# Performance work log

Measured on AMD Instinct MI355X. Metric: run time of the kernel, lower is better.

Reference implementation:

```python
import jax, jax.numpy as jnp
import numpy as np

N = 50000
E = 800000
IN_CH = 128
HID = 16
HEADS = 8
OUT_CH = 64
NEG_SLOPE = 0.2


def _gat_conv(x, src, dst, W, a_src, a_dst, b, heads, ch):
    # x: [N, F_in]; W: [F_in, heads*ch]; a_src/a_dst: [heads, ch]; b: [heads*ch] or [ch]
    n = x.shape[0]
    h = (x @ W).reshape(n, heads, ch)                      # [N, H, C]
    s = jnp.einsum('nhc,hc->nh', h, a_src)                 # [N, H]
    d = jnp.einsum('nhc,hc->nh', h, a_dst)                 # [N, H]
    e = jax.nn.leaky_relu(s[src] + d[dst], NEG_SLOPE)      # [E, H]
    # numerically stable segment softmax over destination neighborhoods
    m = jax.ops.segment_max(e, dst, num_segments=n)        # [N, H]
    m = jnp.where(jnp.isfinite(m), m, 0.0)                 # guard isolated nodes
    w = jnp.exp(e - m[dst])                                # [E, H]
    z = jax.ops.segment_sum(w, dst, num_segments=n)        # [N, H]
    alpha = w / (z[dst] + 1e-16)                           # [E, H]
    msg = h[src] * alpha[:, :, None]                       # [E, H, C]
    out = jax.ops.segment_sum(msg, dst, num_segments=n)    # [N, H, C]
    return out.reshape(n, heads * ch) + b


def setup_inputs() -> dict:
    key = jax.random.key(0)
    ks = jax.random.split(key, 10)
    x = jax.random.normal(ks[0], (N, IN_CH), dtype=jnp.float32)
    edge_index = jax.random.randint(ks[1], (2, E), 0, N, dtype=jnp.int64)
    g1 = 1.0 / np.sqrt(IN_CH)
    g2 = 1.0 / np.sqrt(HEADS * HID)
    W1 = jax.random.normal(ks[2], (IN_CH, HEADS * HID), dtype=jnp.float32) * g1
    a_src1 = jax.random.normal(ks[3], (HEADS, HID), dtype=jnp.float32) * g2
    a_dst1 = jax.random.normal(ks[4], (HEADS, HID), dtype=jnp.float32) * g2
    b1 = jnp.zeros((HEADS * HID,), dtype=jnp.float32)
    W2 = jax.random.normal(ks[5], (HEADS * HID, OUT_CH), dtype=jnp.float32) * g2
    a_src2 = jax.random.normal(ks[6], (1, OUT_CH), dtype=jnp.float32) * (1.0 / np.sqrt(OUT_CH))
    a_dst2 = jax.random.normal(ks[7], (1, OUT_CH), dtype=jnp.float32) * (1.0 / np.sqrt(OUT_CH))
    b2 = jnp.zeros((OUT_CH,), dtype=jnp.float32)
    return {"x": x, "edge_index": edge_index,
            "W1": W1, "a_src1": a_src1, "a_dst1": a_dst1, "b1": b1,
            "W2": W2, "a_src2": a_src2, "a_dst2": a_dst2, "b2": b2}


def reference(x, edge_index, W1, a_src1, a_dst1, b1, W2, a_src2, a_dst2, b2):
    src, dst = edge_index[0], edge_index[1]
    # dropout layers are identity at inference
    h = _gat_conv(x, src, dst, W1, a_src1, a_dst1, b1, HEADS, HID)
    h = jax.nn.elu(h)
    out = _gat_conv(h, src, dst, W2, a_src2, a_dst2, b2, 1, OUT_CH)
    return out
```

## Files before the change

### kernel.cpp

```cpp
#include <hip/hip_runtime.h>
#include <hip/hip_fp16.h>

#define INCH   128
#define HEADS1 8
#define HID1   16
#define C1     128
#define C2     64
#define NEG_SLOPE 0.2f
#define SB     256

using f16x8 = __attribute__((ext_vector_type(8))) _Float16;
using f32x4 = __attribute__((ext_vector_type(4))) float;

__device__ __forceinline__ float lrelu(float v) { return v >= 0.f ? v : NEG_SLOPE * v; }
__device__ __forceinline__ int swzA(int row, int byteInRow) {
  return (row << 8) | (byteInRow ^ ((row & 15) << 4));
}


__global__ void prep_kernel(const float* __restrict__ x, __half* __restrict__ xh,
                            const float* __restrict__ W1, __half* __restrict__ W1t,
                            const float* __restrict__ W2, __half* __restrict__ W2t,
                            const int* __restrict__ dst, int* __restrict__ deg,
                            int cvtB, int tB, int total8, int E) {
  const int b = blockIdx.x, t = threadIdx.x;
  if (b < cvtB) {
    int i = b * 256 + t;
    if (i >= total8) return;
    const float4* p = (const float4*)x + (size_t)i * 2;
    float4 v0 = p[0], v1 = p[1];
    __half2 ha = __floats2half2_rn(v0.x, v0.y);
    __half2 hb = __floats2half2_rn(v0.z, v0.w);
    __half2 hc = __floats2half2_rn(v1.x, v1.y);
    __half2 hd = __floats2half2_rn(v1.z, v1.w);
    uint4 w = { *(unsigned*)&ha, *(unsigned*)&hb, *(unsigned*)&hc, *(unsigned*)&hd };
    ((uint4*)xh)[i] = w;
  } else if (b < cvtB + tB) {
    int id = (b - cvtB) * 256 + t;
    if (id < 128 * 128) {
      int col = id >> 7, k = id & 127;
      W1t[id] = __float2half(W1[k * 128 + col]);
    } else if (id < 128 * 128 + 64 * 128) {
      int idx = id - 128 * 128;
      int col = idx >> 7, k = idx & 127;
      W2t[idx] = __float2half(W2[k * 64 + col]);
    }
  } else {
    int e = (b - cvtB - tB) * 256 + t;
    if (e < E) atomicAdd(&deg[dst[e]], 1);
  }
}


__global__ void scan1_kernel(const int* __restrict__ deg, int* __restrict__ partial, int N) {
  __shared__ int sh[SB];
  const int b = blockIdx.x, t = threadIdx.x;
  const int chunk = (N + SB - 1) / SB;
  const int lo = b * chunk, hi = min(lo + chunk, N);
  int s = 0;
  for (int i = lo + t; i < hi; i += SB) s += deg[i];
  sh[t] = s;
  __syncthreads();
  for (int off = SB / 2; off; off >>= 1) {
    if (t < off) sh[t] += sh[t + off];
    __syncthreads();
  }
  if (t == 0) partial[b] = sh[0];
}

__global__ void scan3_kernel(const int* __restrict__ deg, const int* __restrict__ partial,
                             int* __restrict__ row_start, int N) {
  __shared__ int pref[SB];
  __shared__ int sh[SB];
  const int b = blockIdx.x, t = threadIdx.x;
  int pv = partial[t];
  pref[t] = pv;
  __syncthreads();
  for (int off = 1; off < SB; off <<= 1) {
    int u = (t >= off) ? pref[t - off] : 0;
    __syncthreads();
    pref[t] += u;
    __syncthreads();
  }
  const int chunk = (N + SB - 1) / SB;
  const int lo = b * chunk, hi = min(lo + chunk, N);
  int run = (b == 0) ? 0 : pref[b - 1];
  for (int base = lo; base < hi; base += SB) {
    int i = base + t;
    int v = (i < hi) ? deg[i] : 0;
    sh[t] = v;
    __syncthreads();
    for (int off = 1; off < SB; off <<= 1) {
      int u = (t >= off) ? sh[t - off] : 0;
      __syncthreads();
      sh[t] += u;
      __syncthreads();
    }
    if (i < hi) row_start[i] = run + sh[t] - v;
    run += sh[SB - 1];
    __syncthreads();
  }
  if (b == SB - 1 && t == 0) row_start[N] = run;
}

__global__ void fill_kernel(const int* __restrict__ src, const int* __restrict__ dst,
                            const int* __restrict__ row_start, int* __restrict__ cursor,
                            int* __restrict__ src_sorted, int E) {
  int e = blockIdx.x * blockDim.x + threadIdx.x;
  if (e >= E) return;
  int d = dst[e];
  int slot = row_start[d] + atomicAdd(&cursor[d], 1);
  src_sorted[slot] = src[e];
}

__global__ __launch_bounds__(256) void gemm1_mfma(
    const __half* __restrict__ xh, const __half* __restrict__ W1t,
    const float* __restrict__ a_src, const float* __restrict__ a_dst,
    __half* __restrict__ h1, float* __restrict__ s1, float* __restrict__ d1, int M) {
  __shared__ unsigned char As[16384];
  __shared__ unsigned char Bs[32768];
  const int t = threadIdx.x;
  const int m0 = blockIdx.x * 64;
  for (int c = t; c < 1024; c += 256) {
    int row = c >> 4, seg = c & 15;
    int gr = m0 + row;
    uint4 v = make_uint4(0, 0, 0, 0);
    if (gr < M) v = ((const uint4*)xh)[(unsigned)(gr << 4) + seg];
    *(uint4*)(As + swzA(row, seg << 4)) = v;
  }
  for (int c = t; c < 2048; c += 256) {
    int row = c >> 4, seg = c & 15;
    uint4 v = ((const uint4*)W1t)[(row << 4) + seg];
    *(uint4*)(Bs + swzA(row, seg << 4)) = v;
  }
  __syncthreads();
  const int l = t & 63, wid = t >> 6;
  const int c16 = l & 15;
  const int kOff = (l >> 4) << 4;
  const int rA = (wid << 4) | c16;
  f16x8 a[4];
#pragma unroll
  for (int kb = 0; kb < 4; ++kb)
    a[kb] = *(const f16x8*)(As + swzA(rA, (kb << 6) + kOff));
#pragma unroll
  for (int ct = 0; ct < 8; ++ct) {
    const int rB = (ct << 4) | c16;
    f32x4 acc = {0.f, 0.f, 0.f, 0.f};
#pragma unroll
    for (int kb = 0; kb < 4; ++kb) {
      f16x8 b = *(const f16x8*)(Bs + swzA(rB, (kb << 6) + kOff));
      acc = __builtin_amdgcn_mfma_f32_16x16x32_f16(a[kb], b, acc, 0, 0, 0);
    }
    const int colg = (ct << 4) + c16;
    const float asv = a_src[colg], adv = a_dst[colg];
#pragma unroll
    for (int i = 0; i < 4; ++i) {
      const int n = m0 + (wid << 4) + ((l >> 4) << 2) + i;
      float v = acc[i];
      float sv = v * asv, dv = v * adv;
      sv += __shfl_xor(sv, 1); sv += __shfl_xor(sv, 2);
      sv += __shfl_xor(sv, 4); sv += __shfl_xor(sv, 8);
      dv += __shfl_xor(dv, 1); dv += __shfl_xor(dv, 2);
      dv += __shfl_xor(dv, 4); dv += __shfl_xor(dv, 8);
      if (n < M) {
        h1[(unsigned)(n << 7) + colg] = __float2half(v);
        if (c16 == 0) { s1[n * HEADS1 + ct] = sv; d1[n * HEADS1 + ct] = dv; }
      }
    }
  }
}

__global__ __launch_bounds__(256) void gemm2_mfma(
    const __half* __restrict__ x2h, const __half* __restrict__ W2t,
    const float* __restrict__ a_src, const float* __restrict__ a_dst,
    __half* __restrict__ h2, float* __restrict__ s2, float* __restrict__ d2, int M) {
  __shared__ unsigned char As[16384];
  __shared__ unsigned char Bs[16384];
  const int t = threadIdx.x;
  const int m0 = blockIdx.x * 64;
  for (int c = t; c < 1024; c += 256) {
    int row = c >> 4, seg = c & 15;
    int gr = m0 + row;
    uint4 v = make_uint4(0, 0, 0, 0);
    if (gr < M) v = ((const uint4*)x2h)[(unsigned)(gr << 4) + seg];
    *(uint4*)(As + swzA(row, seg << 4)) = v;
  }
  for (int c = t; c < 1024; c += 256) {
    int row = c >> 4, seg = c & 15;
    uint4 v = ((const uint4*)W2t)[(row << 4) + seg];
    *(uint4*)(Bs + swzA(row, seg << 4)) = v;
  }
  __syncthreads();
  const int l = t & 63, wid = t >> 6;
  const int c16 = l & 15;
  const int kOff = (l >> 4) << 4;
  const int rA = (wid << 4) | c16;
  f16x8 a[4];
#pragma unroll
  for (int kb = 0; kb < 4; ++kb)
    a[kb] = *(const f16x8*)(As + swzA(rA, (kb << 6) + kOff));
  float svp[4] = {0.f, 0.f, 0.f, 0.f};
  float dvp[4] = {0.f, 0.f, 0.f, 0.f};
#pragma unroll
  for (int ct = 0; ct < 4; ++ct) {
    const int rB = (ct << 4) | c16;
    f32x4 acc = {0.f, 0.f, 0.f, 0.f};
#pragma unroll
    for (int kb = 0; kb < 4; ++kb) {
      f16x8 b = *(const f16x8*)(Bs + swzA(rB, (kb << 6) + kOff));
      acc = __builtin_amdgcn_mfma_f32_16x16x32_f16(a[kb], b, acc, 0, 0, 0);
    }
    const int colg = (ct << 4) + c16;
    const float asv = a_src[colg], adv = a_dst[colg];
#pragma unroll
    for (int i = 0; i < 4; ++i) {
      const int n = m0 + (wid << 4) + ((l >> 4) << 2) + i;
      float v = acc[i];
      svp[i] += v * asv;
      dvp[i] += v * adv;
      if (n < M) h2[(unsigned)(n << 6) + colg] = __float2half(v);
    }
  }
#pragma unroll
  for (int i = 0; i < 4; ++i) {
    float sv = svp[i], dv = dvp[i];
    sv += __shfl_xor(sv, 1); sv += __shfl_xor(sv, 2);
    sv += __shfl_xor(sv, 4); sv += __shfl_xor(sv, 8);
    dv += __shfl_xor(dv, 1); dv += __shfl_xor(dv, 2);
    dv += __shfl_xor(dv, 4); dv += __shfl_xor(dv, 8);
    const int n = m0 + (wid << 4) + ((l >> 4) << 2) + i;
    if (c16 == 0 && n < M) { s2[n] = sv; d2[n] = dv; }
  }
}

__global__ __launch_bounds__(256) void layer1_agg(
    const int* __restrict__ row_start, const int* __restrict__ src_sorted,
    const float* __restrict__ s1, const float* __restrict__ d1,
    const __half* __restrict__ h1, const float* __restrict__ b1,
    __half* __restrict__ x2h, int N) {
  __shared__ float wlds[4][64][8];
  const int wv = threadIdx.x >> 6;
  const int lane = threadIdx.x & 63;
  const int le = lane >> 3, h = lane & 7;
  const int es = lane >> 4, cl = lane & 15;
  const int hh = cl >> 1;
  const uint4* __restrict__ h1v = (const uint4*)h1;
  const int waveId = blockIdx.x * 4 + wv;
  const int stride = gridDim.x * 4;
  for (int n = waveId; n < N; n += stride) {
    const int lo = row_start[n], hi = row_start[n + 1];
    const float dv = d1[n * HEADS1 + h];
    float z = 0.f;
    float acc[8] = {0.f, 0.f, 0.f, 0.f, 0.f, 0.f, 0.f, 0.f};
    for (int base = lo; base < hi; base += 64) {
      const int cnt = min(64, hi - base);
      const int c1 = cnt - 1;
      const int ps0 = src_sorted[base + min(es, c1)];
      const int ps1 = src_sorted[base + min(4 + es, c1)];
      const int ps2 = src_sorted[base + min(8 + es, c1)];
      const int ps3 = src_sorted[base + min(12 + es, c1)];
      const uint4 pf0 = h1v[(unsigned)(ps0 << 4) + cl];
      const uint4 pf1 = h1v[(unsigned)(ps1 << 4) + cl];
      const uint4 pf2 = h1v[(unsigned)(ps2 << 4) + cl];
      const uint4 pf3 = h1v[(unsigned)(ps3 << 4) + cl];
      const int rmax = (cnt + 7) >> 3;
      for (int r = 0; r < rmax; ++r) {
        const int j = (r << 3) + le;
        float w = 0.f;
        if (j < cnt) w = __expf(lrelu(s1[src_sorted[base + j] * HEADS1 + h] + dv));
        wlds[wv][j][h] = w;
        z += w;
      }
      {
        const float wA = wlds[wv][es][hh];
        const float wB = wlds[wv][4 + es][hh];
        const __half2* pA = (const __half2*)&pf0;
        const __half2* pB = (const __half2*)&pf1;
#pragma unroll
        for (int k = 0; k < 4; ++k) {
          float2 a2 = __half22float2(pA[k]);
          float2 b2v = __half22float2(pB[k]);
          acc[2 * k]     += wA * a2.x + wB * b2v.x;
          acc[2 * k + 1] += wA * a2.y + wB * b2v.y;
        }
      }
      if (cnt > 8) {
        const float wA = wlds[wv][8 + es][hh];
        const float wB = wlds[wv][12 + es][hh];
        const __half2* pA = (const __half2*)&pf2;
        const __half2* pB = (const __half2*)&pf3;
#pragma unroll
        for (int k = 0; k < 4; ++k) {
          float2 a2 = __half22float2(pA[k]);
          float2 b2v = __half22float2(pB[k]);
          acc[2 * k]     += wA * a2.x + wB * b2v.x;
          acc[2 * k + 1] += wA * a2.y + wB * b2v.y;
        }
      }
      for (int i = 16; i < cnt; i += 8) {
        const int jA = i + es, jB = i + 4 + es;
        const float wA = wlds[wv][jA][hh];
        const float wB = wlds[wv][jB][hh];
        const int sA = src_sorted[base + min(jA, c1)];
        const int sB = src_sorted[base + min(jB, c1)];
        const uint4 fA = h1v[(unsigned)(sA << 4) + cl];
        const uint4 fB = h1v[(unsigned)(sB << 4) + cl];
        const __half2* pA = (const __half2*)&fA;
        const __half2* pB = (const __half2*)&fB;
#pragma unroll
        for (int k = 0; k < 4; ++k) {
          float2 a2 = __half22float2(pA[k]);
          float2 b2v = __half22float2(pB[k]);
          acc[2 * k]     += wA * a2.x + wB * b2v.x;
          acc[2 * k + 1] += wA * a2.y + wB * b2v.y;
        }
      }
    }
    z += __shfl_xor(z, 8); z += __shfl_xor(z, 16); z += __shfl_xor(z, 32);
    const float zsel = __shfl(z, hh);
#pragma unroll
    for (int k = 0; k < 8; ++k) {
      acc[k] += __shfl_xor(acc[k], 16);
      acc[k] += __shfl_xor(acc[k], 32);
    }
    if (es == 0) {
      const float zinv = 1.f / (zsel + 1e-16f);
      __half2 o[4];
#pragma unroll
      for (int k = 0; k < 4; ++k) {
        float ox = acc[2 * k] * zinv + b1[(cl << 3) + 2 * k];
        float oy = acc[2 * k + 1] * zinv + b1[(cl << 3) + 2 * k + 1];
        ox = ox > 0.f ? ox : expm1f(ox);
        oy = oy > 0.f ? oy : expm1f(oy);
        o[k] = __floats2half2_rn(ox, oy);
      }
      ((uint4*)x2h)[(unsigned)(n << 4) + cl] = *(const uint4*)o;
    }
  }
}

__global__ __launch_bounds__(256) void layer2_agg(
    const int* __restrict__ row_start, const int* __restrict__ src_sorted,
    const float* __restrict__ s2, const float* __restrict__ d2,
    const __half* __restrict__ h2, const float* __restrict__ b2,
    float* __restrict__ out, int N) {
  const int wv = threadIdx.x >> 6;
  const int lane = threadIdx.x & 63;
  const int es = lane >> 3, cl = lane & 7;
  const uint4* __restrict__ h2v = (const uint4*)h2;
  const int waveId = blockIdx.x * 4 + wv;
  const int stride = gridDim.x * 4;
  for (int n = waveId; n < N; n += stride) {
    const int lo = row_start[n], hi = row_start[n + 1];
    const float dv = d2[n];
    float z = 0.f;
    float acc[8] = {0.f, 0.f, 0.f, 0.f, 0.f, 0.f, 0.f, 0.f};
    for (int base = lo; base < hi; base += 64) {
      const int cnt = min(64, hi - base);
      const int c1 = cnt - 1;
      const int ps0 = src_sorted[base + min(es, c1)];
      const int ps1 = src_sorted[base + min(8 + es, c1)];
      const int ps2 = src_sorted[base + min(16 + es, c1)];
      const int ps3 = src_sorted[base + min(24 + es, c1)];
      const uint4 pf0 = h2v[(unsigned)(ps0 << 3) + cl];
      const uint4 pf1 = h2v[(unsigned)(ps1 << 3) + cl];
      const uint4 pf2 = h2v[(unsigned)(ps2 << 3) + cl];
      const uint4 pf3 = h2v[(unsigned)(ps3 << 3) + cl];
      float w = 0.f;
      if (lane < cnt) w = __expf(lrelu(s2[src_sorted[base + lane]] + dv));
      z += w;
      {
        const float wA = __shfl(w, es);
        const float wB = __shfl(w, 8 + es);
        const __half2* pA = (const __half2*)&pf0;
        const __half2* pB = (const __half2*)&pf1;
#pragma unroll
        for (int k = 0; k < 4; ++k) {
          float2 a2 = __half22float2(pA[k]);
          float2 b2v = __half22float2(pB[k]);
          acc[2 * k]     += wA * a2.x + wB * b2v.x;
          acc[2 * k + 1] += wA * a2.y + wB * b2v.y;
        }
      }
      if (cnt > 16) {
        const float wA = __shfl(w, 16 + es);
        const float wB = __shfl(w, 24 + es);
        const __half2* pA = (const __half2*)&pf2;
        const __half2* pB = (const __half2*)&pf3;
#pragma unroll
        for (int k = 0; k < 4; ++k) {
          float2 a2 = __half22float2(pA[k]);
          float2 b2v = __half22float2(pB[k]);
          acc[2 * k]     += wA * a2.x + wB * b2v.x;
          acc[2 * k + 1] += wA * a2.y + wB * b2v.y;
        }
      }
      for (int i = 32; i < cnt; i += 16) {
        const int jA = i + es, jB = i + 8 + es;
        const float wA = __shfl(w, jA);
        const float wB = __shfl(w, jB);
        const int sA = src_sorted[base + min(jA, c1)];
        const int sB = src_sorted[base + min(jB, c1)];
        const uint4 fA = h2v[(unsigned)(sA << 3) + cl];
        const uint4 fB = h2v[(unsigned)(sB << 3) + cl];
        const __half2* pA = (const __half2*)&fA;
        const __half2* pB = (const __half2*)&fB;
#pragma unroll
        for (int k = 0; k < 4; ++k) {
          float2 a2 = __half22float2(pA[k]);
          float2 b2v = __half22float2(pB[k]);
          acc[2 * k]     += wA * a2.x + wB * b2v.x;
          acc[2 * k + 1] += wA * a2.y + wB * b2v.y;
        }
      }
    }
#pragma unroll
    for (int off = 1; off < 64; off <<= 1) z += __shfl_xor(z, off);
#pragma unroll
    for (int k = 0; k < 8; ++k) {
      acc[k] += __shfl_xor(acc[k], 8);
      acc[k] += __shfl_xor(acc[k], 16);
      acc[k] += __shfl_xor(acc[k], 32);
    }
    if (es == 0) {
      const float zinv = 1.f / (z + 1e-16f);
      float4 o0, o1;
      o0.x = acc[0] * zinv + b2[(cl << 3) + 0];
      o0.y = acc[1] * zinv + b2[(cl << 3) + 1];
      o0.z = acc[2] * zinv + b2[(cl << 3) + 2];
      o0.w = acc[3] * zinv + b2[(cl << 3) + 3];
      o1.x = acc[4] * zinv + b2[(cl << 3) + 4];
      o1.y = acc[5] * zinv + b2[(cl << 3) + 5];
      o1.z = acc[6] * zinv + b2[(cl << 3) + 6];
      o1.w = acc[7] * zinv + b2[(cl << 3) + 7];
      float4* po = (float4*)&out[(unsigned)(n << 6) + (cl << 3)];
      po[0] = o0;
      po[1] = o1;
    }
  }
}

extern "C" void kernel_launch(void* const* d_in, const int* in_sizes, int n_in,
                              void* d_out, int out_size, void* d_ws, size_t ws_size,
                              hipStream_t stream) {
  const float* x      = (const float*)d_in[0];
  const int*   ei     = (const int*)d_in[1];
  const float* W1     = (const float*)d_in[2];
  const float* a_src1 = (const float*)d_in[3];
  const float* a_dst1 = (const float*)d_in[4];
  const float* b1     = (const float*)d_in[5];
  const float* W2     = (const float*)d_in[6];
  const float* a_src2 = (const float*)d_in[7];
  const float* a_dst2 = (const float*)d_in[8];
  const float* b2     = (const float*)d_in[9];
  float* out = (float*)d_out;

  const int N = in_sizes[0] / INCH;
  const int E = in_sizes[1] / 2;
  const int* src = ei;
  const int* dst = ei + E;

  float* ws = (float*)d_ws;
  size_t o = 0;
  __half* xh  = (__half*)(ws + o); o += (size_t)N * C1 / 2;
  __half* h1  = (__half*)(ws + o); o += (size_t)N * C1 / 2;
  __half* x2h = (__half*)(ws + o); o += (size_t)N * C1 / 2;
  float*  s1  = ws + o;            o += (size_t)N * HEADS1;
  float*  d1  = ws + o;            o += (size_t)N * HEADS1;
  __half* W1t = (__half*)(ws + o); o += 128 * 128 / 2;
  __half* W2t = (__half*)(ws + o); o += 64 * 128 / 2;
  int* deg        = (int*)(ws + o); o += N;
  int* cursor     = (int*)(ws + o); o += N;
  int* row_start  = (int*)(ws + o); o += N + 1;
  int* partial    = (int*)(ws + o); o += SB;
  int* src_sorted = (int*)(ws + o); o += E;
  __half* h2 = h1;
  float*  s2 = (float*)h1 + (size_t)N * 32;
  float*  d2 = s2 + N;

  const int EB = (E + 255) / 256;
  const int NB64 = (N + 63) / 64;
  const int total8 = N * C1 / 8;
  const int cvtB = (total8 + 255) / 256;
  const int tB = (128 * 128 + 64 * 128 + 255) / 256;
  const int histB = EB;
  const int AGGB = min((N + 3) / 4, 2048);

  hipMemsetAsync(deg, 0, (size_t)N * 4, stream);
  hipMemsetAsync(cursor, 0, (size_t)N * 4, stream);

  prep_kernel<<<cvtB + tB + histB, 256, 0, stream>>>(x, xh, W1, W1t, W2, W2t, dst, deg,
                                                     cvtB, tB, total8, E);
  scan1_kernel<<<SB, SB, 0, stream>>>(deg, partial, N);
  scan3_kernel<<<SB, SB, 0, stream>>>(deg, partial, row_start, N);
  fill_kernel<<<EB, 256, 0, stream>>>(src, dst, row_start, cursor, src_sorted, E);

  gemm1_mfma<<<NB64, 256, 0, stream>>>(xh, W1t, a_src1, a_dst1, h1, s1, d1, N);
  layer1_agg<<<AGGB, 256, 0, stream>>>(row_start, src_sorted, s1, d1, h1, b1, x2h, N);

  gemm2_mfma<<<NB64, 256, 0, stream>>>(x2h, W2t, a_src2, a_dst2, h2, s2, d2, N);
  layer2_agg<<<AGGB, 256, 0, stream>>>(row_start, src_sorted, s2, d2, h2, b2, out, N);
}
```

Before: 202.2 us.

## Fuse x fp16 conversion into GEMM1, merge CSR fill with GEMM1, pad rows

The standalone x-to-fp16 conversion pass is removed, and GEMM1 now loads fp32 x and converts it while staging it into LDS. The CSR fill kernel is merged into the GEMM1 launch as extra blocks, and the cursor memset is folded into the scan kernel. Each CSR row is padded to a multiple of 16 entries in a zero-filled src_sorted buffer, which removes the clamp (min) index math in the aggregation kernels. In exchange, an extra memset over the padded buffer is added (roughly 1.6M ints), padded slots gather node 0 with their weights masked, and layer2 drops its second prefetch pair.

```diff
diff --git a/kernel.cpp b/kernel.cpp
--- a/kernel.cpp
+++ b/kernel.cpp
@@ -18,25 +18,13 @@
 }
 
 
-__global__ void prep_kernel(const float* __restrict__ x, __half* __restrict__ xh,
-                            const float* __restrict__ W1, __half* __restrict__ W1t,
+__global__ void prep_kernel(const float* __restrict__ W1, __half* __restrict__ W1t,
                             const float* __restrict__ W2, __half* __restrict__ W2t,
                             const int* __restrict__ dst, int* __restrict__ deg,
-                            int cvtB, int tB, int total8, int E) {
+                            int tB, int E) {
   const int b = blockIdx.x, t = threadIdx.x;
-  if (b < cvtB) {
-    int i = b * 256 + t;
-    if (i >= total8) return;
-    const float4* p = (const float4*)x + (size_t)i * 2;
-    float4 v0 = p[0], v1 = p[1];
-    __half2 ha = __floats2half2_rn(v0.x, v0.y);
-    __half2 hb = __floats2half2_rn(v0.z, v0.w);
-    __half2 hc = __floats2half2_rn(v1.x, v1.y);
-    __half2 hd = __floats2half2_rn(v1.z, v1.w);
-    uint4 w = { *(unsigned*)&ha, *(unsigned*)&hb, *(unsigned*)&hc, *(unsigned*)&hd };
-    ((uint4*)xh)[i] = w;
-  } else if (b < cvtB + tB) {
-    int id = (b - cvtB) * 256 + t;
+  if (b < tB) {
+    int id = b * 256 + t;
     if (id < 128 * 128) {
       int col = id >> 7, k = id & 127;
       W1t[id] = __float2half(W1[k * 128 + col]);
@@ -46,19 +34,23 @@
       W2t[idx] = __float2half(W2[k * 64 + col]);
     }
   } else {
-    int e = (b - cvtB - tB) * 256 + t;
+    int e = (b - tB) * 256 + t;
     if (e < E) atomicAdd(&deg[dst[e]], 1);
   }
 }
 
 
-__global__ void scan1_kernel(const int* __restrict__ deg, int* __restrict__ partial, int N) {
+__global__ void scan1_kernel(const int* __restrict__ deg, int* __restrict__ partial,
+                             int* __restrict__ cursor, int N) {
   __shared__ int sh[SB];
   const int b = blockIdx.x, t = threadIdx.x;
   const int chunk = (N + SB - 1) / SB;
   const int lo = b * chunk, hi = min(lo + chunk, N);
   int s = 0;
-  for (int i = lo + t; i < hi; i += SB) s += deg[i];
+  for (int i = lo + t; i < hi; i += SB) {
+    s += (deg[i] + 15) & ~15;
+    cursor[i] = 0;
+  }
   sh[t] = s;
   __syncthreads();
   for (int off = SB / 2; off; off >>= 1) {
@@ -87,7 +79,7 @@
   int run = (b == 0) ? 0 : pref[b - 1];
   for (int base = lo; base < hi; base += SB) {
     int i = base + t;
-    int v = (i < hi) ? deg[i] : 0;
+    int v = (i < hi) ? ((deg[i] + 15) & ~15) : 0;
     sh[t] = v;
     __syncthreads();
     for (int off = 1; off < SB; off <<= 1) {
@@ -103,29 +95,38 @@
   if (b == SB - 1 && t == 0) row_start[N] = run;
 }
 
-__global__ void fill_kernel(const int* __restrict__ src, const int* __restrict__ dst,
-                            const int* __restrict__ row_start, int* __restrict__ cursor,
-                            int* __restrict__ src_sorted, int E) {
-  int e = blockIdx.x * blockDim.x + threadIdx.x;
-  if (e >= E) return;
-  int d = dst[e];
-  int slot = row_start[d] + atomicAdd(&cursor[d], 1);
-  src_sorted[slot] = src[e];
-}
-
-__global__ __launch_bounds__(256) void gemm1_mfma(
-    const __half* __restrict__ xh, const __half* __restrict__ W1t,
+__global__ __launch_bounds__(256) void combo_kernel(
+    const int* __restrict__ src, const int* __restrict__ dst,
+    const int* __restrict__ row_start, int* __restrict__ cursor,
+    int* __restrict__ src_sorted, int E, int FB,
+    const float* __restrict__ x, const __half* __restrict__ W1t,
     const float* __restrict__ a_src, const float* __restrict__ a_dst,
     __half* __restrict__ h1, float* __restrict__ s1, float* __restrict__ d1, int M) {
   __shared__ unsigned char As[16384];
   __shared__ unsigned char Bs[32768];
   const int t = threadIdx.x;
-  const int m0 = blockIdx.x * 64;
+  if (blockIdx.x < FB) {
+    int e = blockIdx.x * 256 + t;
+    if (e >= E) return;
+    int d = dst[e];
+    int slot = row_start[d] + atomicAdd(&cursor[d], 1);
+    src_sorted[slot] = src[e];
+    return;
+  }
+  const int m0 = (blockIdx.x - FB) * 64;
   for (int c = t; c < 1024; c += 256) {
     int row = c >> 4, seg = c & 15;
     int gr = m0 + row;
     uint4 v = make_uint4(0, 0, 0, 0);
-    if (gr < M) v = ((const uint4*)xh)[(unsigned)(gr << 4) + seg];
+    if (gr < M) {
+      const float4* px = (const float4*)&x[(size_t)gr * 128 + (seg << 3)];
+      float4 v0 = px[0], v1 = px[1];
+      __half2 ha = __floats2half2_rn(v0.x, v0.y);
+      __half2 hb = __floats2half2_rn(v0.z, v0.w);
+      __half2 hc = __floats2half2_rn(v1.x, v1.y);
+      __half2 hd = __floats2half2_rn(v1.z, v1.w);
+      v = make_uint4(*(unsigned*)&ha, *(unsigned*)&hb, *(unsigned*)&hc, *(unsigned*)&hd);
+    }
     *(uint4*)(As + swzA(row, seg << 4)) = v;
   }
   for (int c = t; c < 2048; c += 256) {
@@ -234,7 +235,8 @@
 }
 
 __global__ __launch_bounds__(256) void layer1_agg(
-    const int* __restrict__ row_start, const int* __restrict__ src_sorted,
+    const int* __restrict__ row_start, const int* __restrict__ deg,
+    const int* __restrict__ src_sorted,
     const float* __restrict__ s1, const float* __restrict__ d1,
     const __half* __restrict__ h1, const float* __restrict__ b1,
     __half* __restrict__ x2h, int N) {
@@ -248,17 +250,18 @@
   const int waveId = blockIdx.x * 4 + wv;
   const int stride = gridDim.x * 4;
   for (int n = waveId; n < N; n += stride) {
-    const int lo = row_start[n], hi = row_start[n + 1];
+    const int lo = row_start[n];
+    const int total = deg[n];
     const float dv = d1[n * HEADS1 + h];
     float z = 0.f;
     float acc[8] = {0.f, 0.f, 0.f, 0.f, 0.f, 0.f, 0.f, 0.f};
-    for (int base = lo; base < hi; base += 64) {
-      const int cnt = min(64, hi - base);
-      const int c1 = cnt - 1;
-      const int ps0 = src_sorted[base + min(es, c1)];
-      const int ps1 = src_sorted[base + min(4 + es, c1)];
-      const int ps2 = src_sorted[base + min(8 + es, c1)];
-      const int ps3 = src_sorted[base + min(12 + es, c1)];
+    for (int off0 = 0; off0 < total; off0 += 64) {
+      const int base = lo + off0;
+      const int cnt = min(64, total - off0);
+      const int ps0 = src_sorted[base + es];
+      const int ps1 = src_sorted[base + 4 + es];
+      const int ps2 = src_sorted[base + 8 + es];
+      const int ps3 = src_sorted[base + 12 + es];
       const uint4 pf0 = h1v[(unsigned)(ps0 << 4) + cl];
       const uint4 pf1 = h1v[(unsigned)(ps1 << 4) + cl];
       const uint4 pf2 = h1v[(unsigned)(ps2 << 4) + cl];
@@ -301,8 +304,8 @@
         const int jA = i + es, jB = i + 4 + es;
         const float wA = wlds[wv][jA][hh];
         const float wB = wlds[wv][jB][hh];
-        const int sA = src_sorted[base + min(jA, c1)];
-        const int sB = src_sorted[base + min(jB, c1)];
+        const int sA = src_sorted[base + jA];
+        const int sB = src_sorted[base + jB];
         const uint4 fA = h1v[(unsigned)(sA << 4) + cl];
         const uint4 fB = h1v[(unsigned)(sB << 4) + cl];
         const __half2* pA = (const __half2*)&fA;
@@ -340,7 +343,8 @@
 }
 
 __global__ __launch_bounds__(256) void layer2_agg(
-    const int* __restrict__ row_start, const int* __restrict__ src_sorted,
+    const int* __restrict__ row_start, const int* __restrict__ deg,
+    const int* __restrict__ src_sorted,
     const float* __restrict__ s2, const float* __restrict__ d2,
     const __half* __restrict__ h2, const float* __restrict__ b2,
     float* __restrict__ out, int N) {
@@ -351,21 +355,18 @@
   const int waveId = blockIdx.x * 4 + wv;
   const int stride = gridDim.x * 4;
   for (int n = waveId; n < N; n += stride) {
-    const int lo = row_start[n], hi = row_start[n + 1];
+    const int lo = row_start[n];
+    const int total = deg[n];
     const float dv = d2[n];
     float z = 0.f;
     float acc[8] = {0.f, 0.f, 0.f, 0.f, 0.f, 0.f, 0.f, 0.f};
-    for (int base = lo; base < hi; base += 64) {
-      const int cnt = min(64, hi - base);
-      const int c1 = cnt - 1;
-      const int ps0 = src_sorted[base + min(es, c1)];
-      const int ps1 = src_sorted[base + min(8 + es, c1)];
-      const int ps2 = src_sorted[base + min(16 + es, c1)];
-      const int ps3 = src_sorted[base + min(24 + es, c1)];
+    for (int off0 = 0; off0 < total; off0 += 64) {
+      const int base = lo + off0;
+      const int cnt = min(64, total - off0);
+      const int ps0 = src_sorted[base + es];
+      const int ps1 = src_sorted[base + 8 + es];
       const uint4 pf0 = h2v[(unsigned)(ps0 << 3) + cl];
       const uint4 pf1 = h2v[(unsigned)(ps1 << 3) + cl];
-      const uint4 pf2 = h2v[(unsigned)(ps2 << 3) + cl];
-      const uint4 pf3 = h2v[(unsigned)(ps3 << 3) + cl];
       float w = 0.f;
       if (lane < cnt) w = __expf(lrelu(s2[src_sorted[base + lane]] + dv));
       z += w;
@@ -382,25 +383,12 @@
           acc[2 * k + 1] += wA * a2.y + wB * b2v.y;
         }
       }
-      if (cnt > 16) {
-        const float wA = __shfl(w, 16 + es);
-        const float wB = __shfl(w, 24 + es);
-        const __half2* pA = (const __half2*)&pf2;
-        const __half2* pB = (const __half2*)&pf3;
-#pragma unroll
-        for (int k = 0; k < 4; ++k) {
-          float2 a2 = __half22float2(pA[k]);
-          float2 b2v = __half22float2(pB[k]);
-          acc[2 * k]     += wA * a2.x + wB * b2v.x;
-          acc[2 * k + 1] += wA * a2.y + wB * b2v.y;
-        }
-      }
-      for (int i = 32; i < cnt; i += 16) {
+      for (int i = 16; i < cnt; i += 16) {
         const int jA = i + es, jB = i + 8 + es;
         const float wA = __shfl(w, jA);
         const float wB = __shfl(w, jB);
-        const int sA = src_sorted[base + min(jA, c1)];
-        const int sB = src_sorted[base + min(jB, c1)];
+        const int sA = src_sorted[base + jA];
+        const int sB = src_sorted[base + jB];
         const uint4 fA = h2v[(unsigned)(sA << 3) + cl];
         const uint4 fB = h2v[(unsigned)(sB << 3) + cl];
         const __half2* pA = (const __half2*)&fA;
@@ -459,10 +447,10 @@
   const int E = in_sizes[1] / 2;
   const int* src = ei;
   const int* dst = ei + E;
+  const int EPAD = E + 16 * N;
 
   float* ws = (float*)d_ws;
   size_t o = 0;
-  __half* xh  = (__half*)(ws + o); o += (size_t)N * C1 / 2;
   __half* h1  = (__half*)(ws + o); o += (size_t)N * C1 / 2;
   __half* x2h = (__half*)(ws + o); o += (size_t)N * C1 / 2;
   float*  s1  = ws + o;            o += (size_t)N * HEADS1;
@@ -473,31 +461,28 @@
   int* cursor     = (int*)(ws + o); o += N;
   int* row_start  = (int*)(ws + o); o += N + 1;
   int* partial    = (int*)(ws + o); o += SB;
-  int* src_sorted = (int*)(ws + o); o += E;
+  int* src_sorted = (int*)(ws + o); o += EPAD;
   __half* h2 = h1;
   float*  s2 = (float*)h1 + (size_t)N * 32;
   float*  d2 = s2 + N;
 
   const int EB = (E + 255) / 256;
   const int NB64 = (N + 63) / 64;
-  const int total8 = N * C1 / 8;
-  const int cvtB = (total8 + 255) / 256;
   const int tB = (128 * 128 + 64 * 128 + 255) / 256;
-  const int histB = EB;
   const int AGGB = min((N + 3) / 4, 2048);
 
   hipMemsetAsync(deg, 0, (size_t)N * 4, stream);
-  hipMemsetAsync(cursor, 0, (size_t)N * 4, stream);
-
-  prep_kernel<<<cvtB + tB + histB, 256, 0, stream>>>(x, xh, W1, W1t, W2, W2t, dst, deg,
-                                                     cvtB, tB, total8, E);
-  scan1_kernel<<<SB, SB, 0, stream>>>(deg, partial, N);
+  hipMemsetAsync(src_sorted, 0, (size_t)EPAD * 4, stream);
+
+  prep_kernel<<<tB + EB, 256, 0, stream>>>(W1, W1t, W2, W2t, dst, deg, tB, E);
+  scan1_kernel<<<SB, SB, 0, stream>>>(deg, partial, cursor, N);
   scan3_kernel<<<SB, SB, 0, stream>>>(deg, partial, row_start, N);
-  fill_kernel<<<EB, 256, 0, stream>>>(src, dst, row_start, cursor, src_sorted, E);
-
-  gemm1_mfma<<<NB64, 256, 0, stream>>>(xh, W1t, a_src1, a_dst1, h1, s1, d1, N);
-  layer1_agg<<<AGGB, 256, 0, stream>>>(row_start, src_sorted, s1, d1, h1, b1, x2h, N);
+
+  combo_kernel<<<EB + NB64, 256, 0, stream>>>(src, dst, row_start, cursor, src_sorted,
+                                              E, EB,
+                                              x, W1t, a_src1, a_dst1, h1, s1, d1, N);
+  layer1_agg<<<AGGB, 256, 0, stream>>>(row_start, deg, src_sorted, s1, d1, h1, b1, x2h, N);
 
   gemm2_mfma<<<NB64, 256, 0, stream>>>(x2h, W2t, a_src2, a_dst2, h2, s2, d2, N);
-  layer2_agg<<<AGGB, 256, 0, stream>>>(row_start, src_sorted, s2, d2, h2, b2, out, N);
-}
+  layer2_agg<<<AGGB, 256, 0, stream>>>(row_start, deg, src_sorted, s2, d2, h2, b2, out, N);
+}
```

Measured after the change: 203.6 us. No clear change (+0.7%).
